# Kernel tuning notes

Measured on AMD Instinct MI355X. Metric: run time of the kernel, lower is better.

Reference implementation:

```python
import jax, jax.numpy as jnp
import numpy as np

CUTOFF = 0.5


def setup_inputs() -> dict:
    key = jax.random.key(0)
    k_z, k_d, k_w, k_mu, k_sg = jax.random.split(key, 5)
    N, D_IN, D_OUT = 8192, 128, 128
    z = jax.random.normal(k_z, (N, D_IN), dtype=jnp.float32)
    dist_matrix = jax.random.uniform(k_d, (N, N), dtype=jnp.float32)
    W = jax.random.normal(k_w, (D_IN, D_OUT), dtype=jnp.float32)
    B = jnp.zeros((D_OUT,), dtype=jnp.float32)
    mu = jax.random.normal(k_mu, (1,), dtype=jnp.float32)
    sigma = jax.random.normal(k_sg, (1,), dtype=jnp.float32)
    return {"z": z, "dist_matrix": dist_matrix, "W": W, "B": B, "mu": mu, "sigma": sigma}


def reference(z, dist_matrix, W, B, mu, sigma):
    N = dist_matrix.shape[0]
    # transform every source node once: h[j] = z[j] @ W + B   [N, D_OUT]
    h = z @ W + B
    # pair mask: within cutoff and i != j
    mask = (dist_matrix < CUTOFF) & (~jnp.eye(N, dtype=bool))
    # safe distance to avoid inf/nan where masked out (original skips those pairs)
    r = jnp.where(mask, dist_matrix, 1.0)
    sens = jnp.exp(-(1.0 / r - 1.0 / mu[0]) ** 2 / (2.0 * sigma[0] ** 2))
    S = jnp.where(mask, sens, 0.0)  # [N, N]
    # z_inter[i] = sum_j S[i, j] * h[j]
    return S @ h
```

## Files before the change

### kernel.cpp

```cpp
#include <hip/hip_runtime.h>
#include <hip/hip_bf16.h>

#define NN 8192
#define DD 128
#define BM 16
#define JS 8

typedef __attribute__((ext_vector_type(4))) float f32x4;
typedef __attribute__((ext_vector_type(8))) short bf16x8;
typedef __attribute__((ext_vector_type(4))) unsigned int u32x4;

__device__ __forceinline__ unsigned short f2bf(float x) {
    unsigned u = __float_as_uint(x);
    u += 0x7fffu + ((u >> 16) & 1u);
    return (unsigned short)(u >> 16);
}

__global__ void __launch_bounds__(256) h_transform(
    const float* __restrict__ z, const float* __restrict__ W,
    const float* __restrict__ Bv, unsigned short* __restrict__ hT) {
    __shared__ float zs[BM * DD];
    __shared__ float wt[DD * 132];
    const int t = threadIdx.x;
    const int j0 = blockIdx.x * BM;

    {
        const f32x4* zsrc = (const f32x4*)(z + (size_t)j0 * DD);
        f32x4* zdst = (f32x4*)zs;
        zdst[t] = zsrc[t];
        zdst[t + 256] = zsrc[t + 256];
    }
    for (int q = t; q < DD * 32; q += 256) {
        int k = q >> 5;
        int n0 = (q & 31) << 2;
        f32x4 wv = *(const f32x4*)(W + k * DD + n0);
        wt[(n0 + 0) * 132 + k] = wv[0];
        wt[(n0 + 1) * 132 + k] = wv[1];
        wt[(n0 + 2) * 132 + k] = wv[2];
        wt[(n0 + 3) * 132 + k] = wv[3];
    }
    __syncthreads();

    const int n = t >> 1;
    const int ja = (t & 1) << 3;
    float acc[8];
    float bn = Bv[n];
#pragma unroll
    for (int e = 0; e < 8; e++) acc[e] = bn;

#pragma unroll 8
    for (int k4 = 0; k4 < 32; ++k4) {
        f32x4 wv = *(const f32x4*)&wt[n * 132 + (k4 << 2)];
#pragma unroll
        for (int e = 0; e < 8; e++) {
            f32x4 zv = *(const f32x4*)&zs[(ja + e) * DD + (k4 << 2)];
            acc[e] += zv[0] * wv[0] + zv[1] * wv[1] + zv[2] * wv[2] + zv[3] * wv[3];
        }
    }

    const int j = j0 + ja;
    unsigned short* dst = hT + ((j >> 5) * 4096 + (n >> 4) * 512 +
                                (((j >> 3) & 3) << 7) + ((n & 15) << 3));
    uint4 uv;
    uv.x = (unsigned)f2bf(acc[0]) | ((unsigned)f2bf(acc[1]) << 16);
    uv.y = (unsigned)f2bf(acc[2]) | ((unsigned)f2bf(acc[3]) << 16);
    uv.z = (unsigned)f2bf(acc[4]) | ((unsigned)f2bf(acc[5]) << 16);
    uv.w = (unsigned)f2bf(acc[6]) | ((unsigned)f2bf(acc[7]) << 16);
    *(uint4*)dst = uv;
}

__global__ void __launch_bounds__(64, 2) fused_interact(
    const float* __restrict__ dist, const unsigned short* __restrict__ hT,
    const float* __restrict__ mu, const float* __restrict__ sigma,
    float* __restrict__ part) {
    __shared__ char sfr[8 * 1056];
    const int l = threadIdx.x;
    const int ks = (int)blockIdx.x & 7;
    const int rt = (int)blockIdx.x >> 3;
    const int kbeg = ks * (NN / JS);
    const int r0 = rt * 16;

    const float inv_mu = 1.0f / mu[0];
    const float sg = sigma[0];
    const float ninv2s2 = -1.0f / (2.0f * sg * sg);

    const float* dbase = dist + (size_t)r0 * NN + kbeg + 4 * l;
    const unsigned short* hp = hT + (size_t)(kbeg >> 5) * 4096 + l * 8;

    const int ard = (4 * (l & 15) + (l >> 4)) * 16;
    const int awr = (l >> 3) * 1056 + ((l & 7) >> 1) * 16 + (l & 1) * 8;
    const int colb = kbeg + 4 * l;

    f32x4 acc[8];
#pragma unroll
    for (int f = 0; f < 8; ++f) acc[f] = (f32x4){0.f, 0.f, 0.f, 0.f};

    f32x4 dv[16];
    u32x4 hS[3][8];

#define LDDIST(SC)                                                           \
    do {                                                                     \
        _Pragma("unroll") for (int p = 0; p < 16; ++p)                       \
            dv[p] = *(const f32x4*)(dbase + (size_t)p * NN + (SC) * 256);    \
    } while (0)

#define LDHT(SLOT, KT)                                                       \
    do {                                                                     \
        _Pragma("unroll") for (int f = 0; f < 8; ++f)                        \
            hS[SLOT][f] = *(const u32x4*)(hp + (KT) * 4096 + f * 512);       \
    } while (0)

    LDDIST(0);
    LDHT(0, 0);
    LDHT(1, 1);
    LDHT(2, 2);

#pragma unroll
    for (int sc = 0; sc < 4; ++sc) {
#pragma unroll
        for (int p = 0; p < 16; ++p) {
            const int rg = r0 + p;
            unsigned short hh[4];
#pragma unroll
            for (int e = 0; e < 4; ++e) {
                float d = dv[p][e];
                float qq = __builtin_amdgcn_rcpf(d) - inv_mu;
                float s = __expf(qq * qq * ninv2s2);
                bool keep = (d < 0.5f) & ((colb + sc * 256 + e) != rg);
                hh[e] = f2bf(keep ? s : 0.0f);
            }
            uint2 u;
            u.x = (unsigned)hh[0] | ((unsigned)hh[1] << 16);
            u.y = (unsigned)hh[2] | ((unsigned)hh[3] << 16);
            *(uint2*)(sfr + awr + p * 64) = u;
        }
        if (sc < 3) LDDIST(sc + 1);

#pragma unroll
        for (int g = 0; g < 8; ++g) {
            const int kt = sc * 8 + g;
            bf16x8 a = *(const bf16x8*)(sfr + g * 1056 + ard);
#pragma unroll
            for (int f = 0; f < 8; ++f)
                acc[f] = __builtin_amdgcn_mfma_f32_16x16x32_bf16(
                    a, __builtin_bit_cast(bf16x8, hS[kt % 3][f]), acc[f],
                    0, 0, 0);
            if (kt + 3 < 32) LDHT((kt + 3) % 3, kt + 3);
        }
    }
#undef LDDIST
#undef LDHT

    float* po = part + (size_t)ks * (NN * DD);
    const int orow = r0 + ((l >> 4) << 2);
    const int ocol = l & 15;
#pragma unroll
    for (int f = 0; f < 8; ++f)
#pragma unroll
        for (int rr = 0; rr < 4; ++rr)
            po[(size_t)(orow + rr) * DD + f * 16 + ocol] = acc[f][rr];
}

__global__ void __launch_bounds__(256) reduce_part(
    const float* __restrict__ part, float* __restrict__ outp) {
    const size_t idx = ((size_t)blockIdx.x * 256 + threadIdx.x) << 2;
    f32x4 s = *(const f32x4*)(part + idx);
#pragma unroll
    for (int ksp = 1; ksp < JS; ++ksp)
        s += *(const f32x4*)(part + (size_t)ksp * (NN * DD) + idx);
    *(f32x4*)(outp + idx) = s;
}

extern "C" void kernel_launch(void* const* d_in, const int* in_sizes, int n_in,
                              void* d_out, int out_size, void* d_ws, size_t ws_size,
                              hipStream_t stream) {
    const float* z = (const float*)d_in[0];
    const float* dist = (const float*)d_in[1];
    const float* W = (const float*)d_in[2];
    const float* Bv = (const float*)d_in[3];
    const float* mu = (const float*)d_in[4];
    const float* sigma = (const float*)d_in[5];
    float* out = (float*)d_out;

    unsigned short* hT = (unsigned short*)d_ws;
    const size_t hT_bytes = (size_t)DD * NN * 2;
    float* part = (float*)((char*)d_ws + hT_bytes);

    h_transform<<<NN / BM, 256, 0, stream>>>(z, W, Bv, hT);
    fused_interact<<<(NN / 16) * JS, 64, 0, stream>>>(dist, hT, mu, sigma,
                                                      part);
    reduce_part<<<(NN * DD) / 1024, 256, 0, stream>>>(part, out);
}
```

Baseline: 127.3 us.

## Split fused interaction into separate sensitivity and packed-GEMM kernels over row chunks

Replaces the fused kernel, which computed sensitivities and ran MFMA in the same wavefront, with two kernels. The first writes a bf16 sensitivity matrix into workspace, pre-packed in MFMA fragment order. The second streams those packed fragments together with hT through a register-prefetched MFMA loop. Work is processed in row chunks sized to fit the workspace. The intent is to let each phase run with its own occupancy and memory pattern. In exchange it adds a bf16 NxN write and read through global memory plus extra kernel launches, and the prefetch loop reads past the end of each tile.

```diff
diff --git a/kernel.cpp b/kernel.cpp
--- a/kernel.cpp
+++ b/kernel.cpp
@@ -69,90 +69,106 @@
     *(uint4*)dst = uv;
 }
 
-__global__ void __launch_bounds__(64, 2) fused_interact(
-    const float* __restrict__ dist, const unsigned short* __restrict__ hT,
-    const float* __restrict__ mu, const float* __restrict__ sigma,
-    float* __restrict__ part) {
-    __shared__ char sfr[8 * 1056];
+__global__ void __launch_bounds__(512) sens_stream(
+    const float* __restrict__ dist, const float* __restrict__ mu,
+    const float* __restrict__ sigma, unsigned short* __restrict__ S_pk,
+    int row0) {
+    __shared__ char tile[16 * 2064];
+    const int t = threadIdx.x;
+    const int rb = (int)blockIdx.x >> 3;
+    const int jt = (int)blockIdx.x & 7;
+    const int r0 = row0 + rb * 16;
+    const int jc = jt * 1024;
+
+    const float inv_mu = 1.0f / mu[0];
+    const float sg = sigma[0];
+    const float ninv2s2 = -1.0f / (2.0f * sg * sg);
+
+    const int tr = t >> 5;
+    const int tc = (t & 31) << 2;
+    const float* dp = dist + (size_t)(r0 + tr) * NN + jc + tc;
+    const int rg = r0 + tr;
+
+    f32x4 dv[8];
+#pragma unroll
+    for (int q = 0; q < 8; ++q) dv[q] = *(const f32x4*)(dp + q * 128);
+
+    char* wp = tile + tr * 2064 + tc * 2;
+#pragma unroll
+    for (int q = 0; q < 8; ++q) {
+        unsigned short hh[4];
+#pragma unroll
+        for (int e = 0; e < 4; ++e) {
+            float d = dv[q][e];
+            float qq = __builtin_amdgcn_rcpf(d) - inv_mu;
+            float s = __expf(qq * qq * ninv2s2);
+            bool keep = (d < 0.5f) & ((jc + tc + q * 128 + e) != rg);
+            hh[e] = f2bf(keep ? s : 0.0f);
+        }
+        uint2 u;
+        u.x = (unsigned)hh[0] | ((unsigned)hh[1] << 16);
+        u.y = (unsigned)hh[2] | ((unsigned)hh[3] << 16);
+        *(uint2*)(wp + q * 256) = u;
+    }
+    __syncthreads();
+
+    char* ob = (char*)S_pk + (((size_t)rb * 256 + jt * 32) << 10) + t * 16;
+#pragma unroll
+    for (int p = 0; p < 4; ++p) {
+        const int u = t + 512 * p;
+        const int g = u >> 6;
+        const int l = u & 63;
+        bf16x8 v = *(const bf16x8*)(tile + (l & 15) * 2064 + g * 64 +
+                                    ((l >> 4) << 4));
+        *(bf16x8*)(ob + p * 8192) = v;
+    }
+}
+
+__global__ void __launch_bounds__(64) gemm_pk(
+    const unsigned short* __restrict__ S_pk,
+    const unsigned short* __restrict__ hT, float* __restrict__ part,
+    int row0) {
     const int l = threadIdx.x;
     const int ks = (int)blockIdx.x & 7;
     const int rt = (int)blockIdx.x >> 3;
-    const int kbeg = ks * (NN / JS);
-    const int r0 = rt * 16;
-
-    const float inv_mu = 1.0f / mu[0];
-    const float sg = sigma[0];
-    const float ninv2s2 = -1.0f / (2.0f * sg * sg);
-
-    const float* dbase = dist + (size_t)r0 * NN + kbeg + 4 * l;
-    const unsigned short* hp = hT + (size_t)(kbeg >> 5) * 4096 + l * 8;
-
-    const int ard = (4 * (l & 15) + (l >> 4)) * 16;
-    const int awr = (l >> 3) * 1056 + ((l & 7) >> 1) * 16 + (l & 1) * 8;
-    const int colb = kbeg + 4 * l;
+    const int g0 = ks * 32;
+
+    const char* sp = (const char*)S_pk + (((size_t)rt * 256 + g0) << 10) + l * 16;
+    const unsigned short* hp = hT + (size_t)g0 * 4096 + l * 8;
 
     f32x4 acc[8];
 #pragma unroll
     for (int f = 0; f < 8; ++f) acc[f] = (f32x4){0.f, 0.f, 0.f, 0.f};
 
-    f32x4 dv[16];
+    bf16x8 sA[8];
     u32x4 hS[3][8];
 
-#define LDDIST(SC)                                                           \
-    do {                                                                     \
-        _Pragma("unroll") for (int p = 0; p < 16; ++p)                       \
-            dv[p] = *(const f32x4*)(dbase + (size_t)p * NN + (SC) * 256);    \
-    } while (0)
-
-#define LDHT(SLOT, KT)                                                       \
-    do {                                                                     \
-        _Pragma("unroll") for (int f = 0; f < 8; ++f)                        \
-            hS[SLOT][f] = *(const u32x4*)(hp + (KT) * 4096 + f * 512);       \
-    } while (0)
-
-    LDDIST(0);
-    LDHT(0, 0);
-    LDHT(1, 1);
-    LDHT(2, 2);
-
-#pragma unroll
-    for (int sc = 0; sc < 4; ++sc) {
-#pragma unroll
-        for (int p = 0; p < 16; ++p) {
-            const int rg = r0 + p;
-            unsigned short hh[4];
-#pragma unroll
-            for (int e = 0; e < 4; ++e) {
-                float d = dv[p][e];
-                float qq = __builtin_amdgcn_rcpf(d) - inv_mu;
-                float s = __expf(qq * qq * ninv2s2);
-                bool keep = (d < 0.5f) & ((colb + sc * 256 + e) != rg);
-                hh[e] = f2bf(keep ? s : 0.0f);
-            }
-            uint2 u;
-            u.x = (unsigned)hh[0] | ((unsigned)hh[1] << 16);
-            u.y = (unsigned)hh[2] | ((unsigned)hh[3] << 16);
-            *(uint2*)(sfr + awr + p * 64) = u;
-        }
-        if (sc < 3) LDDIST(sc + 1);
-
-#pragma unroll
-        for (int g = 0; g < 8; ++g) {
-            const int kt = sc * 8 + g;
-            bf16x8 a = *(const bf16x8*)(sfr + g * 1056 + ard);
-#pragma unroll
-            for (int f = 0; f < 8; ++f)
-                acc[f] = __builtin_amdgcn_mfma_f32_16x16x32_bf16(
-                    a, __builtin_bit_cast(bf16x8, hS[kt % 3][f]), acc[f],
-                    0, 0, 0);
-            if (kt + 3 < 32) LDHT((kt + 3) % 3, kt + 3);
-        }
-    }
-#undef LDDIST
-#undef LDHT
+#pragma unroll
+    for (int i = 0; i < 8; ++i)
+        sA[i] = *(const bf16x8*)(sp + i * 1024);
+#pragma unroll
+    for (int j = 0; j < 3; ++j)
+#pragma unroll
+        for (int f = 0; f < 8; ++f)
+            hS[j][f] = *(const u32x4*)(hp + (size_t)j * 4096 + f * 512);
+
+#pragma unroll
+    for (int gg = 0; gg < 32; ++gg) {
+        const int ss = gg & 7;
+        const int hs = gg % 3;
+        bf16x8 a = sA[ss];
+#pragma unroll
+        for (int f = 0; f < 8; ++f)
+            acc[f] = __builtin_amdgcn_mfma_f32_16x16x32_bf16(
+                a, __builtin_bit_cast(bf16x8, hS[hs][f]), acc[f], 0, 0, 0);
+        sA[ss] = *(const bf16x8*)(sp + (gg + 8) * 1024);
+#pragma unroll
+        for (int f = 0; f < 8; ++f)
+            hS[hs][f] = *(const u32x4*)(hp + (size_t)(gg + 3) * 4096 + f * 512);
+    }
 
     float* po = part + (size_t)ks * (NN * DD);
-    const int orow = r0 + ((l >> 4) << 2);
+    const int orow = row0 + rt * 16 + ((l >> 4) << 2);
     const int ocol = l & 15;
 #pragma unroll
     for (int f = 0; f < 8; ++f)
@@ -182,12 +198,25 @@
     const float* sigma = (const float*)d_in[5];
     float* out = (float*)d_out;
 
+    const size_t hT_bytes = (size_t)DD * NN * 2;
+    const size_t part_bytes = (size_t)JS * NN * DD * 4;
+
+    int nq = 4;
+    while (nq < 64 &&
+           hT_bytes + ((size_t)(NN / nq) * NN * 2) + part_bytes > ws_size)
+        nq <<= 1;
+    const int rows = NN / nq;
+    const size_t spk_bytes = (size_t)rows * NN * 2;
+
     unsigned short* hT = (unsigned short*)d_ws;
-    const size_t hT_bytes = (size_t)DD * NN * 2;
-    float* part = (float*)((char*)d_ws + hT_bytes);
+    unsigned short* S_pk = (unsigned short*)((char*)d_ws + hT_bytes);
+    float* part = (float*)((char*)d_ws + hT_bytes + spk_bytes);
 
     h_transform<<<NN / BM, 256, 0, stream>>>(z, W, Bv, hT);
-    fused_interact<<<(NN / 16) * JS, 64, 0, stream>>>(dist, hT, mu, sigma,
-                                                      part);
+    for (int q = 0; q < nq; ++q) {
+        sens_stream<<<(rows / 16) * 8, 512, 0, stream>>>(dist, mu, sigma,
+                                                         S_pk, q * rows);
+        gemm_pk<<<(rows / 16) * 8, 64, 0, stream>>>(S_pk, hT, part, q * rows);
+    }
     reduce_part<<<(NN * DD) / 1024, 256, 0, stream>>>(part, out);
 }
```

New measurement: 152.6 us. +19.9%, slower.

## Restructure interaction kernel into 8-wave blocks with cooperative LDS sensitivity pipeline

Applied to the files above, without the earlier changes.

Replaces the single-wave-per-block design (8 K-split blocks per 16-row tile) with one 512-thread block per row tile. Each of its 8 waves computes sensitivities for 2 rows across a 1024-column chunk and writes them to shared LDS. Every wave then runs MFMAs over its own K-slice of that chunk, writing to its own partial buffer. Distance loads are double-buffered and the next chunk's sensitivity math is software-pipelined behind the MFMAs, with barriers separating phases. This aims to spread exp/rcp work across waves and overlap memory with compute, at the cost of block-level barriers and higher register pressure.

```diff
diff --git a/kernel.cpp b/kernel.cpp
--- a/kernel.cpp
+++ b/kernel.cpp
@@ -5,6 +5,7 @@
 #define DD 128
 #define BM 16
 #define JS 8
+#define GSTR 1040
 
 typedef __attribute__((ext_vector_type(4))) float f32x4;
 typedef __attribute__((ext_vector_type(8))) short bf16x8;
@@ -69,89 +70,130 @@
     *(uint4*)dst = uv;
 }
 
-__global__ void __launch_bounds__(64, 2) fused_interact(
+__global__ void __launch_bounds__(512) fused_interact(
     const float* __restrict__ dist, const unsigned short* __restrict__ hT,
     const float* __restrict__ mu, const float* __restrict__ sigma,
     float* __restrict__ part) {
-    __shared__ char sfr[8 * 1056];
-    const int l = threadIdx.x;
-    const int ks = (int)blockIdx.x & 7;
-    const int rt = (int)blockIdx.x >> 3;
-    const int kbeg = ks * (NN / JS);
-    const int r0 = rt * 16;
+    __shared__ uint4 sfr4[(32 * GSTR) / 16];
+    char* sfr = (char*)sfr4;
+
+    const int t = threadIdx.x;
+    const int w = t >> 6;
+    const int l = t & 63;
+    const int r0 = (int)blockIdx.x * 16;
 
     const float inv_mu = 1.0f / mu[0];
     const float sg = sigma[0];
     const float ninv2s2 = -1.0f / (2.0f * sg * sg);
 
-    const float* dbase = dist + (size_t)r0 * NN + kbeg + 4 * l;
-    const unsigned short* hp = hT + (size_t)(kbeg >> 5) * 4096 + l * 8;
-
-    const int ard = (4 * (l & 15) + (l >> 4)) * 16;
-    const int awr = (l >> 3) * 1056 + ((l & 7) >> 1) * 16 + (l & 1) * 8;
-    const int colb = kbeg + 4 * l;
+    const float* dp0 = dist + (size_t)(r0 + 2 * w) * NN + 4 * l;
+    const float* dp1 = dp0 + NN;
+    const unsigned short* hTb = hT + l * 8;
+
+    const int wbase = (l >> 3) * GSTR + ((l & 7) >> 1) * 256 + (l & 1) * 8 +
+                      (2 * w) * 16;
+    const int abase = (w * 4) * GSTR + l * 16;
 
     f32x4 acc[8];
 #pragma unroll
     for (int f = 0; f < 8; ++f) acc[f] = (f32x4){0.f, 0.f, 0.f, 0.f};
 
-    f32x4 dv[16];
-    u32x4 hS[3][8];
-
-#define LDDIST(SC)                                                           \
-    do {                                                                     \
-        _Pragma("unroll") for (int p = 0; p < 16; ++p)                       \
-            dv[p] = *(const f32x4*)(dbase + (size_t)p * NN + (SC) * 256);    \
-    } while (0)
-
-#define LDHT(SLOT, KT)                                                       \
-    do {                                                                     \
-        _Pragma("unroll") for (int f = 0; f < 8; ++f)                        \
-            hS[SLOT][f] = *(const u32x4*)(hp + (KT) * 4096 + f * 512);       \
-    } while (0)
-
-    LDDIST(0);
-    LDHT(0, 0);
-    LDHT(1, 1);
-    LDHT(2, 2);
-
-#pragma unroll
-    for (int sc = 0; sc < 4; ++sc) {
-#pragma unroll
-        for (int p = 0; p < 16; ++p) {
-            const int rg = r0 + p;
-            unsigned short hh[4];
-#pragma unroll
-            for (int e = 0; e < 4; ++e) {
-                float d = dv[p][e];
-                float qq = __builtin_amdgcn_rcpf(d) - inv_mu;
-                float s = __expf(qq * qq * ninv2s2);
-                bool keep = (d < 0.5f) & ((colb + sc * 256 + e) != rg);
-                hh[e] = f2bf(keep ? s : 0.0f);
-            }
-            uint2 u;
-            u.x = (unsigned)hh[0] | ((unsigned)hh[1] << 16);
-            u.y = (unsigned)hh[2] | ((unsigned)hh[3] << 16);
-            *(uint2*)(sfr + awr + p * 64) = u;
-        }
-        if (sc < 3) LDDIST(sc + 1);
-
-#pragma unroll
-        for (int g = 0; g < 8; ++g) {
-            const int kt = sc * 8 + g;
-            bf16x8 a = *(const bf16x8*)(sfr + g * 1056 + ard);
-#pragma unroll
-            for (int f = 0; f < 8; ++f)
-                acc[f] = __builtin_amdgcn_mfma_f32_16x16x32_bf16(
-                    a, __builtin_bit_cast(bf16x8, hS[kt % 3][f]), acc[f],
-                    0, 0, 0);
-            if (kt + 3 < 32) LDHT((kt + 3) % 3, kt + 3);
-        }
-    }
-#undef LDDIST
-#undef LDHT
-
-    float* po = part + (size_t)ks * (NN * DD);
+    f32x4 dvA[2][4], dvB[2][4];
+    uint2 sv[2][4];
+    u32x4 hb[2][8];
+
+#define LOADDIST(DV, C)                                                      \
+    do {                                                                     \
+        _Pragma("unroll") for (int i_ = 0; i_ < 4; ++i_) {                   \
+            DV[0][i_] = *(const f32x4*)(dp0 + (C) * 1024 + i_ * 256);        \
+            DV[1][i_] = *(const f32x4*)(dp1 + (C) * 1024 + i_ * 256);        \
+        }                                                                    \
+    } while (0)
+
+#define COMPS(DV, C)                                                         \
+    do {                                                                     \
+        _Pragma("unroll") for (int r_ = 0; r_ < 2; ++r_) {                   \
+            const int diag_ = r0 + 2 * w + r_;                               \
+            _Pragma("unroll") for (int i_ = 0; i_ < 4; ++i_) {               \
+                unsigned short hh[4];                                        \
+                _Pragma("unroll") for (int e_ = 0; e_ < 4; ++e_) {           \
+                    float d = DV[r_][i_][e_];                                \
+                    float qq = __builtin_amdgcn_rcpf(d) - inv_mu;            \
+                    float s = __expf(qq * qq * ninv2s2);                     \
+                    bool keep = (d < 0.5f) &                                 \
+                                (((C) * 1024 + i_ * 256 + 4 * l + e_) !=     \
+                                 diag_);                                     \
+                    hh[e_] = f2bf(keep ? s : 0.0f);                          \
+                }                                                            \
+                sv[r_][i_].x = (unsigned)hh[0] | ((unsigned)hh[1] << 16);    \
+                sv[r_][i_].y = (unsigned)hh[2] | ((unsigned)hh[3] << 16);    \
+            }                                                                \
+        }                                                                    \
+    } while (0)
+
+#define WRITES()                                                             \
+    do {                                                                     \
+        _Pragma("unroll") for (int r_ = 0; r_ < 2; ++r_)                     \
+            _Pragma("unroll") for (int i_ = 0; i_ < 4; ++i_)                 \
+                *(uint2*)(sfr + wbase + i_ * (8 * GSTR) + r_ * 16) =         \
+                    sv[r_][i_];                                              \
+    } while (0)
+
+#define HTISS(GI, C)                                                         \
+    do {                                                                     \
+        const unsigned short* hp_ =                                          \
+            hTb + ((C) * 32 + w * 4 + (GI)) * 4096;                          \
+        _Pragma("unroll") for (int f_ = 0; f_ < 8; ++f_)                     \
+            hb[(GI) & 1][f_] = *(const u32x4*)(hp_ + f_ * 512);              \
+    } while (0)
+
+#define MFMAG(GI)                                                            \
+    do {                                                                     \
+        bf16x8 a_ = *(const bf16x8*)(sfr + abase + (GI) * GSTR);             \
+        _Pragma("unroll") for (int f_ = 0; f_ < 8; ++f_)                     \
+            acc[f_] = __builtin_amdgcn_mfma_f32_16x16x32_bf16(               \
+                a_, __builtin_bit_cast(bf16x8, hb[(GI) & 1][f_]), acc[f_],   \
+                0, 0, 0);                                                    \
+    } while (0)
+
+#define BODY(C, DVF, DVH)                                                    \
+    do {                                                                     \
+        WRITES();                                                            \
+        asm volatile("s_waitcnt lgkmcnt(0)" ::: "memory");                   \
+        __builtin_amdgcn_s_barrier();                                        \
+        HTISS(0, C);                                                         \
+        HTISS(1, C);                                                         \
+        MFMAG(0);                                                            \
+        HTISS(2, C);                                                         \
+        MFMAG(1);                                                            \
+        HTISS(3, C);                                                         \
+        MFMAG(2);                                                            \
+        MFMAG(3);                                                            \
+        __builtin_amdgcn_sched_barrier(0);                                   \
+        COMPS(DVH, (C) + 1);                                                 \
+        __builtin_amdgcn_sched_barrier(0);                                   \
+        LOADDIST(DVF, ((C) + 2) & 7);                                        \
+        asm volatile("" ::: "memory");                                       \
+        __builtin_amdgcn_s_barrier();                                        \
+    } while (0)
+
+    LOADDIST(dvA, 0);
+    LOADDIST(dvB, 1);
+    COMPS(dvA, 0);
+
+#pragma unroll 1
+    for (int c = 0; c < 8; c += 2) {
+        BODY(c, dvA, dvB);
+        BODY(c + 1, dvB, dvA);
+    }
+#undef LOADDIST
+#undef COMPS
+#undef WRITES
+#undef HTISS
+#undef MFMAG
+#undef BODY
+
+    float* po = part + (size_t)w * (NN * DD);
     const int orow = r0 + ((l >> 4) << 2);
     const int ocol = l & 15;
 #pragma unroll
@@ -187,7 +229,6 @@
     float* part = (float*)((char*)d_ws + hT_bytes);
 
     h_transform<<<NN / BM, 256, 0, stream>>>(z, W, Bv, hT);
-    fused_interact<<<(NN / 16) * JS, 64, 0, stream>>>(dist, hT, mu, sigma,
-                                                      part);
+    fused_interact<<<NN / 16, 512, 0, stream>>>(dist, hT, mu, sigma, part);
     reduce_part<<<(NN * DD) / 1024, 256, 0, stream>>>(part, out);
 }
```

Result: slower. 145.1 us (+14.0%).
